# Kernel optimization log

Hardware: AMD Instinct MI355X
Metric: run time of the kernel (lower is better)

## Reference

```python
import jax, jax.numpy as jnp
import numpy as np

B = 2048
N_USERS = 100000
N_ITEMS = 50000
N = N_USERS + N_ITEMS
EMB = 64
NNZ = 100000


def setup_inputs() -> dict:
    key = jax.random.key(0)
    k1, k2, k3, k4 = jax.random.split(key, 4)
    u_id = jax.random.randint(k1, (B,), 0, N_USERS, dtype=jnp.int64 if jax.config.jax_enable_x64 else jnp.int32)
    pos_i_id = jax.random.randint(k2, (B,), 0, N, dtype=u_id.dtype)
    train_mask = jax.random.randint(k3, (2, NNZ), 0, B, dtype=u_id.dtype)
    all_embed = jax.random.normal(k4, (N, EMB), dtype=jnp.float32)
    return {"u_id": u_id, "pos_i_id": pos_i_id, "train_mask": train_mask, "all_embed": all_embed}


def reference(u_id, pos_i_id, train_mask, all_embed):
    # policy_type == 'uij': scores = (u_e + pos_e) @ all_e^T  -> [B, N]
    u_e = all_embed[u_id]
    pos_e = all_embed[pos_i_id]
    scores = jnp.einsum("bd,nd->bn", u_e + pos_e, all_embed)
    # Note: the original computes a sparse train-mask tensor (sp_mask) but never
    # uses it; only the zero->-inf masking below affects the output.
    logits = jnp.where(scores == 0.0, -jnp.inf, scores)
    probs = jax.nn.softmax(logits, axis=1)  # [B, N]
    # Categorical sampling per row (fixed key for reproducibility)
    samples = jax.random.categorical(jax.random.key(42), logits, axis=1)  # [B]
    selected_neg_prob = jnp.take_along_axis(probs, samples[:, None], axis=1)[:, 0]
    return samples, selected_neg_prob
```

## Files before the change

kernel.cpp:

```cpp
#include <hip/hip_runtime.h>
#include <stdint.h>

#define B_ROWS   2048
#define N_COLS   150000
#define NSTRIPS  128
#define CHUNK    128
#define NCHUNK   1172
#define ROWG     16

#define NEG_HUGE (-3.0e38f)
#define G_SPAN_HARD  20.6f
#define G_MAX_MARGIN 15.944f
#define EPS_B        2.0e-4f
#define G_FILTER_SLACK 3e-5f

#define LOG2E_F 1.44269504088896340736f
#define LN2_F   0.69314718055994530942f

#if __has_builtin(__builtin_amdgcn_exp2f)
#define EXP2F(x) __builtin_amdgcn_exp2f(x)
#else
#define EXP2F(x) exp2f(x)
#endif

#define WS_MPART 0
#define WS_ZPART (B_ROWS * NSTRIPS)
#define WS_CMAX  (2 * B_ROWS * NSTRIPS)
#define WS_M     (WS_CMAX + B_ROWS * NCHUNK)
#define WS_Z     (WS_M + B_ROWS)
#define WS_VLB   (WS_Z + B_ROWS)
#define WS_CSTAR (WS_VLB + B_ROWS)
#define WS_BEST  (WS_CSTAR + B_ROWS)
#define WS_ENORM (WS_BEST + 2 * B_ROWS)
#define WS_QNORM (WS_ENORM + 2048)
#define WS_EHI   (WS_QNORM + B_ROWS)
#define WS_ELO   (WS_EHI + NCHUNK * 4096)
#define WS_END   (WS_ELO + NCHUNK * 4096)

typedef __attribute__((ext_vector_type(8))) unsigned short ushort8;
typedef __attribute__((ext_vector_type(8))) short short8;
typedef __attribute__((ext_vector_type(4))) float f32x4;

__device__ __forceinline__ uint32_t rotl32(uint32_t x, int r) {
  return (x << r) | (x >> (32 - r));
}

__device__ __forceinline__ void threefry2x32_k42(uint32_t& x0, uint32_t& x1) {
  const uint32_t ks0 = 0u;
  const uint32_t ks1 = 42u;
  const uint32_t ks2 = 0x1BD11BDAu ^ 0u ^ 42u;
  x0 += ks0; x1 += ks1;
#define TF_R(r) { x0 += x1; x1 = rotl32(x1, (r)); x1 ^= x0; }
  TF_R(13) TF_R(15) TF_R(26) TF_R(6)
  x0 += ks1; x1 += ks2 + 1u;
  TF_R(17) TF_R(29) TF_R(16) TF_R(24)
  x0 += ks2; x1 += ks0 + 2u;
  TF_R(13) TF_R(15) TF_R(26) TF_R(6)
  x0 += ks0; x1 += ks1 + 3u;
  TF_R(17) TF_R(29) TF_R(16) TF_R(24)
  x0 += ks1; x1 += ks2 + 4u;
  TF_R(13) TF_R(15) TF_R(26) TF_R(6)
  x0 += ks2; x1 += ks0 + 5u;
#undef TF_R
}

__device__ __forceinline__ float gumbel_from_bits(uint32_t bits) {
  const uint32_t mant = bits >> 9;
  const float f = __uint_as_float(mant | 0x3f800000u) - 1.0f;
  const float l1 = mant ? log1pf(f - 1.0f) : -87.33654475055311f;
  return -__logf(-l1);
}

__device__ __forceinline__ float gumbel_at(uint32_t flat_idx) {
  uint32_t x0 = 0u, x1 = flat_idx;
  threefry2x32_k42(x0, x1);
  return gumbel_from_bits(x0 ^ x1);
}

__device__ __forceinline__ unsigned long long pack_vn(float v, int n) {
  uint32_t u = __float_as_uint(v);
  u ^= ((uint32_t)((int32_t)u >> 31)) | 0x80000000u;
  return ((unsigned long long)u << 32) | (uint32_t)(0xFFFFFFFFu - (uint32_t)n);
}

__device__ __forceinline__ float unpack_v(unsigned long long p) {
  uint32_t u = (uint32_t)(p >> 32);
  u = (u & 0x80000000u) ? (u ^ 0x80000000u) : ~u;
  return __uint_as_float(u);
}

__device__ __forceinline__ int unpack_n(unsigned long long p) {
  return (int)(0xFFFFFFFFu - (uint32_t)(p & 0xFFFFFFFFull));
}

__device__ __forceinline__ unsigned long long umax64(unsigned long long a,
                                                     unsigned long long b) {
  return a > b ? a : b;
}

__device__ __forceinline__ float dot_q_e(const float4* q4, const float4* e4) {
  float s = 0.0f;
#pragma unroll
  for (int k4 = 0; k4 < 16; ++k4) {
    const float4 e = e4[k4];
    const float4 q = q4[k4];
    s = fmaf(q.x, e.x, s);
    s = fmaf(q.y, e.y, s);
    s = fmaf(q.z, e.z, s);
    s = fmaf(q.w, e.w, s);
  }
  return s;
}

__device__ __forceinline__ unsigned short f32_to_bf16_rne(float f) {
  const uint32_t u = __float_as_uint(f);
  return (unsigned short)((u + 0x7fffu + ((u >> 16) & 1u)) >> 16);
}
__device__ __forceinline__ float bf16_to_f32(unsigned short h) {
  return __uint_as_float(((uint32_t)h) << 16);
}

__global__ __launch_bounds__(256) void advnet_enorm(const float* __restrict__ emb,
                                                    float* __restrict__ ws) {
  const int c = blockIdx.x;
  const int t = threadIdx.x;
  const int lane = t & 63;
  const int row = t >> 1;
  const int n = c * CHUNK + row;
  float ss = 0.0f;
  if (n < N_COLS) {
    const float4* p = (const float4*)emb + (size_t)n * 16 + (t & 1) * 8;
#pragma unroll
    for (int i = 0; i < 8; ++i) {
      const float4 v = p[i];
      ss = fmaf(v.x, v.x, ss); ss = fmaf(v.y, v.y, ss);
      ss = fmaf(v.z, v.z, ss); ss = fmaf(v.w, v.w, ss);
    }
  }
  ss += __shfl_xor(ss, 1, 64);
  float mx = ss;
  for (int off = 2; off < 64; off <<= 1) mx = fmaxf(mx, __shfl_xor(mx, off, 64));
  __shared__ float sm[4];
  if (lane == 0) sm[t >> 6] = mx;
  __syncthreads();
  if (t == 0)
    ws[WS_ENORM + c] =
        sqrtf(fmaxf(fmaxf(sm[0], sm[1]), fmaxf(sm[2], sm[3]))) * 1.00002f;
}

__global__ __launch_bounds__(256) void advnet_ebuild(const float* __restrict__ emb,
                                                     float* __restrict__ ws) {
  const int c = blockIdx.x;
  const int t = threadIdx.x;
  char* hi_b = (char*)(ws + WS_EHI) + (size_t)c * 16384;
  char* lo_b = (char*)(ws + WS_ELO) + (size_t)c * 16384;
  float mx = 0.0f;
#pragma unroll
  for (int k = 0; k < 4; ++k) {
    const int j = t + 256 * k;
    const int row = j >> 3, kq = j & 7;
    const int n = c * CHUNK + row;
    ushort8 hi = (ushort8)0, lo = (ushort8)0;
    float ss = 0.0f;
    if (n < N_COLS) {
      const float4* ep = (const float4*)emb + (size_t)n * 16 + kq * 2;
      const float4 a0 = ep[0], a1 = ep[1];
      const float e[8] = {a0.x, a0.y, a0.z, a0.w, a1.x, a1.y, a1.z, a1.w};
#pragma unroll
      for (int j8 = 0; j8 < 8; ++j8) {
        const unsigned short h = f32_to_bf16_rne(e[j8]);
        hi[j8] = h;
        lo[j8] = f32_to_bf16_rne(e[j8] - bf16_to_f32(h));
        ss = fmaf(e[j8], e[j8], ss);
      }
    }
    const int gz = kq ^ (row & 7);
    *(ushort8*)(hi_b + (size_t)(row * 8 + gz) * 16) = hi;
    *(ushort8*)(lo_b + (size_t)(row * 8 + gz) * 16) = lo;
    ss += __shfl_xor(ss, 1, 64);
    ss += __shfl_xor(ss, 2, 64);
    ss += __shfl_xor(ss, 4, 64);
    mx = fmaxf(mx, ss);
  }
  for (int off = 8; off < 64; off <<= 1) mx = fmaxf(mx, __shfl_xor(mx, off, 64));
  __shared__ float sm[4];
  if ((t & 63) == 0) sm[t >> 6] = mx;
  __syncthreads();
  if (t == 0)
    ws[WS_ENORM + c] =
        sqrtf(fmaxf(fmaxf(sm[0], sm[1]), fmaxf(sm[2], sm[3]))) * 1.00002f;
}

__device__ __forceinline__ void stage_tbl(const char* tb_hi, const char* tb_lo,
                                          unsigned short* eh, unsigned short* el,
                                          int c, int wave, int lane) {
  const size_t cb = (size_t)c * 16384 + (size_t)(wave * 1024 + lane * 16);
  const int wo = wave * 1024;
#pragma unroll
  for (int i = 0; i < 4; ++i) {
    const int off = i * 4096;
    __builtin_amdgcn_global_load_lds(
        (const __attribute__((address_space(1))) void*)(tb_hi + cb + off),
        (__attribute__((address_space(3))) void*)((char*)eh + wo + off), 16, 0, 0);
    __builtin_amdgcn_global_load_lds(
        (const __attribute__((address_space(1))) void*)(tb_lo + cb + off),
        (__attribute__((address_space(3))) void*)((char*)el + wo + off), 16, 0, 0);
  }
}

__device__ __forceinline__ void stage_conv(const float* __restrict__ emb,
                                           unsigned short* eh, unsigned short* el,
                                           int c, int tid) {
  const int n0 = c * CHUNK;
#pragma unroll
  for (int k = 0; k < 4; ++k) {
    const int p = tid + 256 * k;
    const int row = p >> 3, kq = p & 7;
    const int n = n0 + row;
    ushort8 hi = (ushort8)0, lo = (ushort8)0;
    if (n < N_COLS) {
      const float4* ep = (const float4*)emb + (size_t)n * 16 + kq * 2;
      const float4 a0 = ep[0], a1 = ep[1];
      const float e[8] = {a0.x, a0.y, a0.z, a0.w, a1.x, a1.y, a1.z, a1.w};
#pragma unroll
      for (int j = 0; j < 8; ++j) {
        const unsigned short h = f32_to_bf16_rne(e[j]);
        hi[j] = h;
        lo[j] = f32_to_bf16_rne(e[j] - bf16_to_f32(h));
      }
    }
    const int off = row * 64 + ((kq * 8) ^ ((row & 7) << 3));
    *(ushort8*)&eh[off] = hi;
    *(ushort8*)&el[off] = lo;
  }
}

template <bool TBL>
__global__ __launch_bounds__(256, 2) void advnet_gemm(
    const int* __restrict__ u_id, const int* __restrict__ pos_id,
    const float* __restrict__ emb, float* __restrict__ ws) {
  __shared__ unsigned short eh_s[8192], el_s[8192];

  const int tid = threadIdx.x;
  const int raw = blockIdx.x;
  const int b8 = raw & 7;
  const int rest = raw >> 3;
  const int rg = rest & 15;
  const int strip = b8 + 8 * (rest >> 4);
  const int wave = tid >> 6;
  const int lane = tid & 63;
  const int lc = lane & 15;
  const int lg = lane >> 4;

#pragma unroll
  for (int k = 0; k < 4; ++k) {
    const int p = tid + 256 * k;
    const int row = p >> 3, kq = p & 7;
    const int b = rg * 128 + row;
    const float4* ua = (const float4*)emb + (size_t)u_id[b] * 16 + kq * 2;
    const float4* pa = (const float4*)emb + (size_t)pos_id[b] * 16 + kq * 2;
    const float4 a0 = ua[0], a1 = ua[1], c0 = pa[0], c1 = pa[1];
    const float q[8] = {(a0.x + c0.x) * LOG2E_F, (a0.y + c0.y) * LOG2E_F,
                        (a0.z + c0.z) * LOG2E_F, (a0.w + c0.w) * LOG2E_F,
                        (a1.x + c1.x) * LOG2E_F, (a1.y + c1.y) * LOG2E_F,
                        (a1.z + c1.z) * LOG2E_F, (a1.w + c1.w) * LOG2E_F};
    ushort8 hi, lo;
#pragma unroll
    for (int j = 0; j < 8; ++j) {
      const unsigned short h = f32_to_bf16_rne(q[j]);
      hi[j] = h;
      lo[j] = f32_to_bf16_rne(q[j] - bf16_to_f32(h));
    }
    const int off = row * 64 + ((kq * 8) ^ ((row & 7) << 3));
    *(ushort8*)&eh_s[off] = hi;
    *(ushort8*)&el_s[off] = lo;
  }
  __syncthreads();

  short8 qh_r[2][2], ql_r[2][2];
#pragma unroll
  for (int kh = 0; kh < 2; ++kh)
#pragma unroll
    for (int rt = 0; rt < 2; ++rt) {
      const int r = wave * 32 + rt * 16 + lc;
      const int off = r * 64 + (((kh * 4 + lg) * 8) ^ ((r & 7) << 3));
      qh_r[kh][rt] = *(const short8*)&eh_s[off];
      ql_r[kh][rt] = *(const short8*)&el_s[off];
    }
  __syncthreads();

  float m[8], Z[8];
#pragma unroll
  for (int s = 0; s < 8; ++s) { m[s] = NEG_HUGE; Z[s] = 0.0f; }

  const char* tb_hi = (const char*)(ws + WS_EHI);
  const char* tb_lo = (const char*)(ws + WS_ELO);

  for (int c = strip; c < NCHUNK; c += NSTRIPS) {
    if (TBL) stage_tbl(tb_hi, tb_lo, eh_s, el_s, c, wave, lane);
    else     stage_conv(emb, eh_s, el_s, c, tid);
    __syncthreads();

    f32x4 acc[2][8];
#pragma unroll
    for (int rt = 0; rt < 2; ++rt)
#pragma unroll
      for (int ct = 0; ct < 8; ++ct) acc[rt][ct] = (f32x4){0.f, 0.f, 0.f, 0.f};

#pragma unroll
    for (int kh = 0; kh < 2; ++kh) {
#pragma unroll
      for (int ct = 0; ct < 8; ++ct) {
        const int col = ct * 16 + lc;
        const int off = col * 64 + (((kh * 4 + lg) * 8) ^ ((col & 7) << 3));
        const short8 ehf = *(const short8*)&eh_s[off];
        const short8 elf = *(const short8*)&el_s[off];
#pragma unroll
        for (int rt = 0; rt < 2; ++rt) {
          acc[rt][ct] = __builtin_amdgcn_mfma_f32_16x16x32_bf16(qh_r[kh][rt], ehf, acc[rt][ct], 0, 0, 0);
          acc[rt][ct] = __builtin_amdgcn_mfma_f32_16x16x32_bf16(qh_r[kh][rt], elf, acc[rt][ct], 0, 0, 0);
          acc[rt][ct] = __builtin_amdgcn_mfma_f32_16x16x32_bf16(ql_r[kh][rt], ehf, acc[rt][ct], 0, 0, 0);
        }
      }
    }

#pragma unroll
    for (int rt = 0; rt < 2; ++rt) {
#pragma unroll
      for (int j = 0; j < 4; ++j) {
        const int s = rt * 4 + j;
        float cm = acc[rt][0][j];
#pragma unroll
        for (int ct = 1; ct < 8; ++ct) cm = fmaxf(cm, acc[rt][ct][j]);
        const float nm = fmaxf(m[s], cm);
        float za = 0.0f;
#pragma unroll
        for (int ct = 0; ct < 8; ++ct) za += EXP2F(acc[rt][ct][j] - nm);
        Z[s] = Z[s] * EXP2F(m[s] - nm) + za;
        m[s] = nm;
        float cr = cm;
        cr = fmaxf(cr, __shfl_xor(cr, 1, 64));
        cr = fmaxf(cr, __shfl_xor(cr, 2, 64));
        cr = fmaxf(cr, __shfl_xor(cr, 4, 64));
        cr = fmaxf(cr, __shfl_xor(cr, 8, 64));
        if (lc == 0) {
          const int row = rg * 128 + wave * 32 + rt * 16 + lg * 4 + j;
          ws[WS_CMAX + (size_t)row * NCHUNK + c] = cr;
        }
      }
    }
    __syncthreads();
  }

#pragma unroll
  for (int rt = 0; rt < 2; ++rt) {
#pragma unroll
    for (int j = 0; j < 4; ++j) {
      const int s = rt * 4 + j;
      float mi = m[s], Zi = Z[s];
      for (int off = 1; off < 16; off <<= 1) {
        const float om = __shfl_xor(mi, off, 64);
        const float oZ = __shfl_xor(Zi, off, 64);
        const float nm = fmaxf(mi, om);
        Zi = Zi * EXP2F(mi - nm) + oZ * EXP2F(om - nm);
        mi = nm;
      }
      if (lc == 0) {
        const int row = rg * 128 + wave * 32 + rt * 16 + lg * 4 + j;
        ws[WS_MPART + (size_t)row * NSTRIPS + strip] = mi;
        ws[WS_ZPART + (size_t)row * NSTRIPS + strip] = Zi;
      }
    }
  }
}

__global__ __launch_bounds__(128) void advnet_rowstat(
    const int* __restrict__ u_id, const int* __restrict__ pos_id,
    const float* __restrict__ emb, float* __restrict__ ws) {
  const int r = blockIdx.x;
  const int t = threadIdx.x;

  __shared__ float sA[2], sB[2];
  __shared__ unsigned long long sP[2];
  __shared__ float qrow[64];

  const size_t idx = (size_t)r * NSTRIPS + t;
  const float ms = ws[WS_MPART + idx];
  const float zs = ws[WS_ZPART + idx];
  float Ms = ms;
  for (int off = 1; off < 64; off <<= 1) Ms = fmaxf(Ms, __shfl_xor(Ms, off, 64));
  if ((t & 63) == 0) sA[t >> 6] = Ms;
  __syncthreads();
  Ms = fmaxf(sA[0], sA[1]);
  float z = zs * EXP2F(ms - Ms);
  for (int off = 1; off < 64; off <<= 1) z += __shfl_xor(z, off, 64);
  if ((t & 63) == 0) sB[t >> 6] = z;
  __syncthreads();
  const float Z = sB[0] + sB[1];
  const float M_nat = Ms * LN2_F;

  unsigned long long cp = 0ull;
  for (int c = t; c < NCHUNK; c += 128)
    cp = umax64(cp, pack_vn(ws[WS_CMAX + (size_t)r * NCHUNK + c], c));
  for (int off = 1; off < 64; off <<= 1)
    cp = umax64(cp, __shfl_xor(cp, off, 64));
  if ((t & 63) == 0) sP[t >> 6] = cp;
  __syncthreads();
  cp = umax64(sP[0], sP[1]);
  const int cstar = unpack_n(cp);

  if (t < 16) {
    const float4 a = ((const float4*)emb)[(size_t)u_id[r] * 16 + t];
    const float4 c = ((const float4*)emb)[(size_t)pos_id[r] * 16 + t];
    ((float4*)qrow)[t] = make_float4(a.x + c.x, a.y + c.y, a.z + c.z, a.w + c.w);
  }
  __syncthreads();

  {
    const float qv = qrow[t & 63];
    float ss = qv * qv;
    for (int off = 1; off < 64; off <<= 1) ss += __shfl_xor(ss, off, 64);
    if (t == 0) ws[WS_QNORM + r] = sqrtf(ss) * 1.00002f;
  }

  unsigned long long bp = 0ull;
  const int n = cstar * CHUNK + t;
  if (n < N_COLS) {
    const float s = dot_q_e((const float4*)qrow, (const float4*)emb + (size_t)n * 16);
    if (s != 0.0f && s >= M_nat - G_SPAN_HARD) {
      const uint32_t L = (uint32_t)r * (uint32_t)N_COLS + (uint32_t)n;
      bp = pack_vn(gumbel_at(L) + s, n);
    }
  }
  for (int off = 1; off < 64; off <<= 1)
    bp = umax64(bp, __shfl_xor(bp, off, 64));
  if ((t & 63) == 0) sP[t >> 6] = bp;
  __syncthreads();
  if (t == 0) {
    const unsigned long long best = umax64(sP[0], sP[1]);
    ((unsigned long long*)(ws + WS_BEST))[r] = best;
    ws[WS_VLB + r] = unpack_v(best);
    ws[WS_M + r] = M_nat;
    ws[WS_Z + r] = Z;
    ((int*)ws)[WS_CSTAR + r] = cstar;
  }
}

#define SVCAP 2048
__global__ __launch_bounds__(256) void advnet_pick(
    const int* __restrict__ u_id, const int* __restrict__ pos_id,
    const float* __restrict__ emb, float* __restrict__ ws) {
  const int r = blockIdx.x >> 1;
  const int par = blockIdx.x & 1;
  const int t = threadIdx.x;

  __shared__ float qrow[64];
  __shared__ unsigned short cq[600];
  __shared__ float cqg[600];
  __shared__ unsigned int svpk[SVCAP];
  __shared__ float svg[SVCAP];
  __shared__ int cqn, svn;
  __shared__ unsigned long long sred[4];

  if (t == 0) { cqn = 0; svn = 0; }
  if (t < 16) {
    const float4 a = ((const float4*)emb)[(size_t)u_id[r] * 16 + t];
    const float4 c = ((const float4*)emb)[(size_t)pos_id[r] * 16 + t];
    ((float4*)qrow)[t] = make_float4(a.x + c.x, a.y + c.y, a.z + c.z, a.w + c.w);
  }
  const float vlb = ws[WS_VLB + r];
  const float bq = ws[WS_QNORM + r] * EPS_B;
  const int cstar = ((const int*)ws)[WS_CSTAR + r];
  __syncthreads();

  for (int c = par + 2 * t; c < NCHUNK; c += 512) {
    if (c == cstar) continue;
    const float cm = ws[WS_CMAX + (size_t)r * NCHUNK + c];
    const float gth = vlb - fmaf(cm, LN2_F, bq * ws[WS_ENORM + c]);
    if (gth < G_MAX_MARGIN) {
      const int k = atomicAdd(&cqn, 1);
      cq[k] = (unsigned short)c;
      cqg[k] = gth;
    }
  }
  __syncthreads();
  const int nq = cqn;
  const float4* qr4 = (const float4*)qrow;

  unsigned long long bp = 0ull;

  for (int base = 0; base < nq; base += 8) {
    if (svn > SVCAP - 1024) {
      __syncthreads();
      const int cnt = svn;
      for (int k = t; k < cnt; k += 256) {
        const int n = (int)svpk[k];
        const float s = dot_q_e(qr4, (const float4*)emb + (size_t)n * 16);
        if (s != 0.0f) bp = umax64(bp, pack_vn(svg[k] + s, n));
      }
      __syncthreads();
      if (t == 0) svn = 0;
      __syncthreads();
    }
#pragma unroll
    for (int u = 0; u < 4; ++u) {
      const int idx = t + 256 * u;
      const int slot = base + (idx >> 7);
      if (slot < nq) {
        const int n = (int)cq[slot] * CHUNK + (idx & 127);
        if (n < N_COLS) {
          const float g = gumbel_at((uint32_t)r * (uint32_t)N_COLS + (uint32_t)n);
          if (g > cqg[slot] - G_FILTER_SLACK) {
            const int k = atomicAdd(&svn, 1);
            if (k < SVCAP) { svpk[k] = (unsigned)n; svg[k] = g; }
          }
        }
      }
    }
    __syncthreads();
  }

  {
    const int cnt = svn < SVCAP ? svn : SVCAP;
    for (int k = t; k < cnt; k += 256) {
      const int n = (int)svpk[k];
      const float s = dot_q_e(qr4, (const float4*)emb + (size_t)n * 16);
      if (s != 0.0f) bp = umax64(bp, pack_vn(svg[k] + s, n));
    }
  }

  for (int off = 1; off < 64; off <<= 1)
    bp = umax64(bp, __shfl_xor(bp, off, 64));
  if ((t & 63) == 0) sred[t >> 6] = bp;
  __syncthreads();
  if (t == 0) {
    const unsigned long long b =
        umax64(umax64(sred[0], sred[1]), umax64(sred[2], sred[3]));
    if (b) atomicMax((unsigned long long*)(ws + WS_BEST) + r, b);
  }
}

__global__ __launch_bounds__(64) void advnet_final(
    const int* __restrict__ u_id, const int* __restrict__ pos_id,
    const float* __restrict__ emb, const float* __restrict__ ws,
    float* __restrict__ out) {
  const int r = blockIdx.x * 64 + threadIdx.x;
  if (r >= B_ROWS) return;
  const unsigned long long w = ((const unsigned long long*)(ws + WS_BEST))[r];
  const int n = unpack_n(w);
  const float4* qa = (const float4*)emb + (size_t)u_id[r] * 16;
  const float4* qb = (const float4*)emb + (size_t)pos_id[r] * 16;
  const float4* e4 = (const float4*)emb + (size_t)n * 16;
  float s = 0.0f;
#pragma unroll
  for (int k4 = 0; k4 < 16; ++k4) {
    const float4 a = qa[k4], b = qb[k4], e = e4[k4];
    float4 q;
    q.x = a.x + b.x; q.y = a.y + b.y; q.z = a.z + b.z; q.w = a.w + b.w;
    s = fmaf(q.x, e.x, s);
    s = fmaf(q.y, e.y, s);
    s = fmaf(q.z, e.z, s);
    s = fmaf(q.w, e.w, s);
  }
  out[r] = (float)n;
  out[B_ROWS + r] = __expf(s - ws[WS_M + r]) / ws[WS_Z + r];
}

extern "C" void kernel_launch(void* const* d_in, const int* in_sizes, int n_in,
                              void* d_out, int out_size, void* d_ws, size_t ws_size,
                              hipStream_t stream) {
  const int* u_id = (const int*)d_in[0];
  const int* pos_id = (const int*)d_in[1];
  const float* emb = (const float*)d_in[3];
  float* ws = (float*)d_ws;
  float* out = (float*)d_out;

  const size_t need = (size_t)WS_END * 4;
  const bool tbl = ws_size >= need;

  if (tbl) {
    advnet_ebuild<<<dim3(NCHUNK), dim3(256), 0, stream>>>(emb, ws);
    advnet_gemm<true><<<dim3(ROWG * NSTRIPS), dim3(256), 0, stream>>>(
        u_id, pos_id, emb, ws);
  } else {
    advnet_enorm<<<dim3(NCHUNK), dim3(256), 0, stream>>>(emb, ws);
    advnet_gemm<false><<<dim3(ROWG * NSTRIPS), dim3(256), 0, stream>>>(
        u_id, pos_id, emb, ws);
  }
  advnet_rowstat<<<dim3(B_ROWS), dim3(128), 0, stream>>>(u_id, pos_id, emb, ws);
  advnet_pick<<<dim3(B_ROWS * 2), dim3(256), 0, stream>>>(u_id, pos_id, emb, ws);
  advnet_final<<<dim3(B_ROWS / 64), dim3(64), 0, stream>>>(u_id, pos_id, emb, ws, out);
}
```

Before: 258.6 us.

## Fuse rowstat and final into pick kernel, defer online-softmax rescaling in GEMM

```diff
diff --git a/kernel.cpp b/kernel.cpp
--- a/kernel.cpp
+++ b/kernel.cpp
@@ -13,6 +13,7 @@
 #define G_MAX_MARGIN 15.944f
 #define EPS_B        2.0e-4f
 #define G_FILTER_SLACK 3e-5f
+#define DEFER_THR_LOG2 12.0f
 
 #define LOG2E_F 1.44269504088896340736f
 #define LN2_F   0.69314718055994530942f
@@ -29,8 +30,8 @@
 #define WS_M     (WS_CMAX + B_ROWS * NCHUNK)
 #define WS_Z     (WS_M + B_ROWS)
 #define WS_VLB   (WS_Z + B_ROWS)
-#define WS_CSTAR (WS_VLB + B_ROWS)
-#define WS_BEST  (WS_CSTAR + B_ROWS)
+#define WS_DONE  (WS_VLB + B_ROWS)
+#define WS_BEST  (WS_DONE + B_ROWS)
 #define WS_ENORM (WS_BEST + 2 * B_ROWS)
 #define WS_QNORM (WS_ENORM + 2048)
 #define WS_EHI   (WS_QNORM + B_ROWS)
@@ -332,12 +333,14 @@
         float cm = acc[rt][0][j];
 #pragma unroll
         for (int ct = 1; ct < 8; ++ct) cm = fmaxf(cm, acc[rt][ct][j]);
-        const float nm = fmaxf(m[s], cm);
+        if (cm > m[s] + DEFER_THR_LOG2) {
+          Z[s] *= EXP2F(m[s] - cm);
+          m[s] = cm;
+        }
         float za = 0.0f;
 #pragma unroll
-        for (int ct = 0; ct < 8; ++ct) za += EXP2F(acc[rt][ct][j] - nm);
-        Z[s] = Z[s] * EXP2F(m[s] - nm) + za;
-        m[s] = nm;
+        for (int ct = 0; ct < 8; ++ct) za += EXP2F(acc[rt][ct][j] - m[s]);
+        Z[s] += za;
         float cr = cm;
         cr = fmaxf(cr, __shfl_xor(cr, 1, 64));
         cr = fmaxf(cr, __shfl_xor(cr, 2, 64));
@@ -374,93 +377,25 @@
   }
 }
 
-__global__ __launch_bounds__(128) void advnet_rowstat(
-    const int* __restrict__ u_id, const int* __restrict__ pos_id,
-    const float* __restrict__ emb, float* __restrict__ ws) {
-  const int r = blockIdx.x;
-  const int t = threadIdx.x;
-
-  __shared__ float sA[2], sB[2];
-  __shared__ unsigned long long sP[2];
-  __shared__ float qrow[64];
-
-  const size_t idx = (size_t)r * NSTRIPS + t;
-  const float ms = ws[WS_MPART + idx];
-  const float zs = ws[WS_ZPART + idx];
-  float Ms = ms;
-  for (int off = 1; off < 64; off <<= 1) Ms = fmaxf(Ms, __shfl_xor(Ms, off, 64));
-  if ((t & 63) == 0) sA[t >> 6] = Ms;
-  __syncthreads();
-  Ms = fmaxf(sA[0], sA[1]);
-  float z = zs * EXP2F(ms - Ms);
-  for (int off = 1; off < 64; off <<= 1) z += __shfl_xor(z, off, 64);
-  if ((t & 63) == 0) sB[t >> 6] = z;
-  __syncthreads();
-  const float Z = sB[0] + sB[1];
-  const float M_nat = Ms * LN2_F;
-
-  unsigned long long cp = 0ull;
-  for (int c = t; c < NCHUNK; c += 128)
-    cp = umax64(cp, pack_vn(ws[WS_CMAX + (size_t)r * NCHUNK + c], c));
-  for (int off = 1; off < 64; off <<= 1)
-    cp = umax64(cp, __shfl_xor(cp, off, 64));
-  if ((t & 63) == 0) sP[t >> 6] = cp;
-  __syncthreads();
-  cp = umax64(sP[0], sP[1]);
-  const int cstar = unpack_n(cp);
-
-  if (t < 16) {
-    const float4 a = ((const float4*)emb)[(size_t)u_id[r] * 16 + t];
-    const float4 c = ((const float4*)emb)[(size_t)pos_id[r] * 16 + t];
-    ((float4*)qrow)[t] = make_float4(a.x + c.x, a.y + c.y, a.z + c.z, a.w + c.w);
-  }
-  __syncthreads();
-
-  {
-    const float qv = qrow[t & 63];
-    float ss = qv * qv;
-    for (int off = 1; off < 64; off <<= 1) ss += __shfl_xor(ss, off, 64);
-    if (t == 0) ws[WS_QNORM + r] = sqrtf(ss) * 1.00002f;
-  }
-
-  unsigned long long bp = 0ull;
-  const int n = cstar * CHUNK + t;
-  if (n < N_COLS) {
-    const float s = dot_q_e((const float4*)qrow, (const float4*)emb + (size_t)n * 16);
-    if (s != 0.0f && s >= M_nat - G_SPAN_HARD) {
-      const uint32_t L = (uint32_t)r * (uint32_t)N_COLS + (uint32_t)n;
-      bp = pack_vn(gumbel_at(L) + s, n);
-    }
-  }
-  for (int off = 1; off < 64; off <<= 1)
-    bp = umax64(bp, __shfl_xor(bp, off, 64));
-  if ((t & 63) == 0) sP[t >> 6] = bp;
-  __syncthreads();
-  if (t == 0) {
-    const unsigned long long best = umax64(sP[0], sP[1]);
-    ((unsigned long long*)(ws + WS_BEST))[r] = best;
-    ws[WS_VLB + r] = unpack_v(best);
-    ws[WS_M + r] = M_nat;
-    ws[WS_Z + r] = Z;
-    ((int*)ws)[WS_CSTAR + r] = cstar;
-  }
-}
-
 #define SVCAP 2048
 __global__ __launch_bounds__(256) void advnet_pick(
     const int* __restrict__ u_id, const int* __restrict__ pos_id,
-    const float* __restrict__ emb, float* __restrict__ ws) {
+    const float* __restrict__ emb, float* __restrict__ ws,
+    float* __restrict__ out) {
   const int r = blockIdx.x >> 1;
   const int par = blockIdx.x & 1;
   const int t = threadIdx.x;
+  const int lane = t & 63;
+  const int w = t >> 6;
 
   __shared__ float qrow[64];
+  __shared__ float sA[4], sB[4];
+  __shared__ unsigned long long sP[4];
   __shared__ unsigned short cq[600];
   __shared__ float cqg[600];
   __shared__ unsigned int svpk[SVCAP];
   __shared__ float svg[SVCAP];
   __shared__ int cqn, svn;
-  __shared__ unsigned long long sred[4];
 
   if (t == 0) { cqn = 0; svn = 0; }
   if (t < 16) {
@@ -468,10 +403,59 @@
     const float4 c = ((const float4*)emb)[(size_t)pos_id[r] * 16 + t];
     ((float4*)qrow)[t] = make_float4(a.x + c.x, a.y + c.y, a.z + c.z, a.w + c.w);
   }
-  const float vlb = ws[WS_VLB + r];
-  const float bq = ws[WS_QNORM + r] * EPS_B;
-  const int cstar = ((const int*)ws)[WS_CSTAR + r];
-  __syncthreads();
+
+  float ms = NEG_HUGE, zs = 0.0f;
+  if (t < 128) {
+    ms = ws[WS_MPART + (size_t)r * NSTRIPS + t];
+    zs = ws[WS_ZPART + (size_t)r * NSTRIPS + t];
+  }
+  float vv = ms;
+  for (int off = 1; off < 64; off <<= 1) vv = fmaxf(vv, __shfl_xor(vv, off, 64));
+  if (lane == 0) sA[w] = vv;
+  __syncthreads();
+  const float Ms = fmaxf(fmaxf(sA[0], sA[1]), fmaxf(sA[2], sA[3]));
+  const float M_nat = Ms * LN2_F;
+
+  float z = zs * EXP2F(ms - Ms);
+  for (int off = 1; off < 64; off <<= 1) z += __shfl_xor(z, off, 64);
+  if (lane == 0) sB[w] = z;
+
+  unsigned long long cp = 0ull;
+  for (int c = t; c < NCHUNK; c += 256)
+    cp = umax64(cp, pack_vn(ws[WS_CMAX + (size_t)r * NCHUNK + c], c));
+  for (int off = 1; off < 64; off <<= 1) cp = umax64(cp, __shfl_xor(cp, off, 64));
+  if (lane == 0) sP[w] = cp;
+  __syncthreads();
+  const float Zr = sB[0] + sB[1] + sB[2] + sB[3];
+  cp = umax64(umax64(sP[0], sP[1]), umax64(sP[2], sP[3]));
+  const int cstar = unpack_n(cp);
+
+  if (t < 64) {
+    const float qv = qrow[t];
+    float ss = qv * qv;
+    for (int off = 1; off < 64; off <<= 1) ss += __shfl_xor(ss, off, 64);
+    if (t == 0) sA[0] = sqrtf(ss) * 1.00002f;
+  }
+
+  unsigned long long bps = 0ull;
+  if (t < 128) {
+    const int n = cstar * CHUNK + t;
+    if (n < N_COLS) {
+      const float s = dot_q_e((const float4*)qrow, (const float4*)emb + (size_t)n * 16);
+      if (s != 0.0f && s >= M_nat - G_SPAN_HARD) {
+        const uint32_t L = (uint32_t)r * (uint32_t)N_COLS + (uint32_t)n;
+        bps = pack_vn(gumbel_at(L) + s, n);
+      }
+    }
+  }
+  unsigned long long bs = bps;
+  for (int off = 1; off < 64; off <<= 1) bs = umax64(bs, __shfl_xor(bs, off, 64));
+  if (lane == 0) sP[w] = bs;
+  __syncthreads();
+  const unsigned long long seed =
+      umax64(umax64(sP[0], sP[1]), umax64(sP[2], sP[3]));
+  const float vlb = unpack_v(seed);
+  const float bq = sA[0] * EPS_B;
 
   for (int c = par + 2 * t; c < NCHUNK; c += 512) {
     if (c == cstar) continue;
@@ -529,41 +513,26 @@
     }
   }
 
-  for (int off = 1; off < 64; off <<= 1)
-    bp = umax64(bp, __shfl_xor(bp, off, 64));
-  if ((t & 63) == 0) sred[t >> 6] = bp;
+  for (int off = 1; off < 64; off <<= 1) bp = umax64(bp, __shfl_xor(bp, off, 64));
+  if (lane == 0) sP[w] = bp;
   __syncthreads();
   if (t == 0) {
-    const unsigned long long b =
-        umax64(umax64(sred[0], sred[1]), umax64(sred[2], sred[3]));
-    if (b) atomicMax((unsigned long long*)(ws + WS_BEST) + r, b);
-  }
-}
-
-__global__ __launch_bounds__(64) void advnet_final(
-    const int* __restrict__ u_id, const int* __restrict__ pos_id,
-    const float* __restrict__ emb, const float* __restrict__ ws,
-    float* __restrict__ out) {
-  const int r = blockIdx.x * 64 + threadIdx.x;
-  if (r >= B_ROWS) return;
-  const unsigned long long w = ((const unsigned long long*)(ws + WS_BEST))[r];
-  const int n = unpack_n(w);
-  const float4* qa = (const float4*)emb + (size_t)u_id[r] * 16;
-  const float4* qb = (const float4*)emb + (size_t)pos_id[r] * 16;
-  const float4* e4 = (const float4*)emb + (size_t)n * 16;
-  float s = 0.0f;
-#pragma unroll
-  for (int k4 = 0; k4 < 16; ++k4) {
-    const float4 a = qa[k4], b = qb[k4], e = e4[k4];
-    float4 q;
-    q.x = a.x + b.x; q.y = a.y + b.y; q.z = a.z + b.z; q.w = a.w + b.w;
-    s = fmaf(q.x, e.x, s);
-    s = fmaf(q.y, e.y, s);
-    s = fmaf(q.z, e.z, s);
-    s = fmaf(q.w, e.w, s);
-  }
-  out[r] = (float)n;
-  out[B_ROWS + r] = __expf(s - ws[WS_M + r]) / ws[WS_Z + r];
+    unsigned long long tot =
+        umax64(umax64(sP[0], sP[1]), umax64(sP[2], sP[3]));
+    tot = umax64(tot, seed);
+    unsigned long long* bestp = (unsigned long long*)(ws + WS_BEST) + r;
+    atomicMax(bestp, tot);
+    __threadfence();
+    int* done = (int*)(ws + WS_DONE);
+    if (atomicAdd(&done[r], 1) == 1) {
+      __threadfence();
+      const unsigned long long wb = atomicMax(bestp, 0ull);
+      const int nw = unpack_n(wb);
+      const float s = dot_q_e(qr4, (const float4*)emb + (size_t)nw * 16);
+      out[r] = (float)nw;
+      out[B_ROWS + r] = EXP2F(fmaf(s, LOG2E_F, -Ms)) / Zr;
+    }
+  }
 }
 
 extern "C" void kernel_launch(void* const* d_in, const int* in_sizes, int n_in,
@@ -578,6 +547,8 @@
   const size_t need = (size_t)WS_END * 4;
   const bool tbl = ws_size >= need;
 
+  hipMemsetAsync((void*)(ws + WS_DONE), 0, (size_t)(3 * B_ROWS) * 4, stream);
+
   if (tbl) {
     advnet_ebuild<<<dim3(NCHUNK), dim3(256), 0, stream>>>(emb, ws);
     advnet_gemm<true><<<dim3(ROWG * NSTRIPS), dim3(256), 0, stream>>>(
@@ -587,7 +558,5 @@
     advnet_gemm<false><<<dim3(ROWG * NSTRIPS), dim3(256), 0, stream>>>(
         u_id, pos_id, emb, ws);
   }
-  advnet_rowstat<<<dim3(B_ROWS), dim3(128), 0, stream>>>(u_id, pos_id, emb, ws);
-  advnet_pick<<<dim3(B_ROWS * 2), dim3(256), 0, stream>>>(u_id, pos_id, emb, ws);
-  advnet_final<<<dim3(B_ROWS / 64), dim3(64), 0, stream>>>(u_id, pos_id, emb, ws, out);
-}
+  advnet_pick<<<dim3(B_ROWS * 2), dim3(256), 0, stream>>>(u_id, pos_id, emb, ws, out);
+}
```

New measurement: 421.4 us. +63.0%, slower.
